# Kernel tuning notes

Hardware: AMD Instinct MI355X
Metric: run time of the kernel (lower is better)

Reference implementation:

```python
import jax, jax.numpy as jnp
import numpy as np


def _gelu(x):
    return jax.nn.gelu(x, approximate=False)


def _conv2d(x, w, b, pad=0, dil=1, groups=1):
    y = jax.lax.conv_general_dilated(
        x, w, (1, 1), [(pad, pad), (pad, pad)], rhs_dilation=(dil, dil),
        dimension_numbers=('NCHW', 'OIHW', 'NCHW'), feature_group_count=groups)
    return y + b[None, :, None, None]


def _ln_last(x, g, b, eps=1e-5):
    m = jnp.mean(x, -1, keepdims=True)
    v = jnp.var(x, -1, keepdims=True)
    return (x - m) * jax.lax.rsqrt(v + eps) * g + b


def _ln2d(x, g, b, eps=1e-5):
    # LayerNorm over channel dim of NCHW
    m = jnp.mean(x, 1, keepdims=True)
    v = jnp.var(x, 1, keepdims=True)
    return (x - m) * jax.lax.rsqrt(v + eps) * g[None, :, None, None] + b[None, :, None, None]


def _bilinear(x, py, px):
    # x: [B,C,H,W]; py,px: [B,H,W] float sample coords; zero outside
    B, C, H, W = x.shape
    y0 = jnp.floor(py)
    x0 = jnp.floor(px)
    wy = py - y0
    wx = px - x0
    xf = x.reshape(B, C, H * W)

    def g(yi, xi):
        valid = ((yi >= 0) & (yi < H) & (xi >= 0) & (xi < W)).astype(x.dtype)
        yc = jnp.clip(yi, 0, H - 1).astype(jnp.int32)
        xc = jnp.clip(xi, 0, W - 1).astype(jnp.int32)
        idx = (yc * W + xc).reshape(B, 1, H * W)
        v = jnp.take_along_axis(xf, idx, axis=2).reshape(B, C, H, W)
        return v * valid[:, None]

    return (g(y0, x0) * ((1 - wy) * (1 - wx))[:, None]
            + g(y0, x0 + 1) * ((1 - wy) * wx)[:, None]
            + g(y0 + 1, x0) * (wy * (1 - wx))[:, None]
            + g(y0 + 1, x0 + 1) * (wy * wx)[:, None])


def _deform_dw(x, ow, ob, w, b, dil):
    # modulated deformable depthwise 3x3 conv, offset_groups=1
    B, C, H, W = x.shape
    pad = dil
    off = _conv2d(x, ow, ob, pad=pad, dil=dil)          # [B,27,H,W]
    ox, oy, m = jnp.split(off, 3, axis=1)               # each [B,9,H,W]
    m = jax.nn.sigmoid(m)
    ys = jnp.arange(H, dtype=x.dtype)[None, :, None]
    xs = jnp.arange(W, dtype=x.dtype)[None, None, :]
    acc = jnp.zeros_like(x)
    for ki in range(3):
        for kj in range(3):
            kk = ki * 3 + kj
            py = ys - pad + ki * dil + oy[:, kk]
            px = xs - pad + kj * dil + ox[:, kk]
            s = _bilinear(x, py, px)                    # [B,C,H,W]
            acc = acc + s * m[:, kk][:, None] * w[:, 0, ki, kj][None, :, None, None]
    return acc + b[None, :, None, None]


def _forward(image_embed, inter_prototypes, intra_prototypes, masks,
             proj_w, proj_b, lin_w, lin_b, tok_g, tok_b, alpha,
             in_w, in_b, off0_w, off0_b, dw0_w, dw0_b,
             off1_w, off1_b, dw1_w, dw1_b, cv_w, cv_b, ln_g, ln_b,
             op0_w, op0_b, op1_w, op1_b, op2_w, op2_b,
             out0_w, out0_b, out1_w, out1_b):
    C = image_embed.shape[1]
    scale = C ** -0.5
    # prototype tokens [B,Q,C]
    pt = jnp.einsum('bqc,bnc->bqn', inter_prototypes, intra_prototypes)
    t = jnp.concatenate([inter_prototypes, pt], axis=-1) @ proj_w + proj_b
    t = _gelu(t) @ lin_w + lin_b
    t = _ln_last(t, tok_g, tok_b)
    # mask gating of image features
    pe = jnp.einsum('bnc,bnhw->bchw', intra_prototypes, masks)
    img = image_embed * pe + image_embed
    # DeformAttn
    x = _gelu(_conv2d(img, in_w, in_b))
    a = _deform_dw(x, off0_w, off0_b, dw0_w, dw0_b, dil=1)
    a = _deform_dw(a, off1_w, off1_b, dw1_w, dw1_b, dil=3)
    a = _conv2d(a, cv_w, cv_b)
    x = x * a + img
    x = _ln2d(x, ln_g, ln_b)
    y = _conv2d(x, op0_w, op0_b)
    y = _gelu(_conv2d(y, op1_w, op1_b, pad=1, groups=C))
    y = _conv2d(y, op2_w, op2_b)
    dense = y + x
    # prototype cross-attention over 8 tokens
    attn = jnp.einsum('bchw,bqc->bqhw', dense, t) * scale
    attn = jax.nn.softmax(attn, axis=1)
    attn = jnp.einsum('bqhw,bqc->bchw', attn, t)
    attn = attn + dense * alpha[None, :, None, None]
    o = _gelu(_conv2d(attn, out0_w, out0_b))
    o = _conv2d(o, out1_w, out1_b)
    return o


def setup_inputs():
    key = jax.random.key(0)
    ks = jax.random.split(key, 40)
    B, C, H, W, Q, N = 16, 256, 64, 64, 8, 9
    f32 = jnp.float32

    def rn(k, shp, s=1.0):
        return jax.random.normal(k, shp, f32) * s

    inp = {
        'image_embed': rn(ks[0], (B, C, H, W)),
        'inter_prototypes': rn(ks[1], (B, Q, C)),
        'intra_prototypes': rn(ks[2], (B, N, C)),
        'masks': jax.random.uniform(ks[3], (B, N, H, W), f32),
        'proj_w': rn(ks[4], (C + N, C), 0.02), 'proj_b': jnp.zeros((C,), f32),
        'lin_w': rn(ks[5], (C, C), 0.02), 'lin_b': jnp.zeros((C,), f32),
        'tok_g': 1.0 + rn(ks[6], (C,), 0.05), 'tok_b': rn(ks[7], (C,), 0.05),
        'alpha': jnp.ones((C,), f32) * 0.001,
        'in_w': rn(ks[8], (C, C, 1, 1), 0.02), 'in_b': jnp.zeros((C,), f32),
        'off0_w': rn(ks[9], (27, C, 3, 3), 0.01), 'off0_b': rn(ks[10], (27,), 0.01),
        'dw0_w': rn(ks[11], (C, 1, 3, 3), 0.2), 'dw0_b': jnp.zeros((C,), f32),
        'off1_w': rn(ks[12], (27, C, 3, 3), 0.01), 'off1_b': rn(ks[13], (27,), 0.01),
        'dw1_w': rn(ks[14], (C, 1, 3, 3), 0.2), 'dw1_b': jnp.zeros((C,), f32),
        'cv_w': rn(ks[15], (C, C, 1, 1), 0.02), 'cv_b': jnp.zeros((C,), f32),
        'ln_g': 1.0 + rn(ks[16], (C,), 0.05), 'ln_b': rn(ks[17], (C,), 0.05),
        'op0_w': rn(ks[18], (C, C, 1, 1), 0.02), 'op0_b': jnp.zeros((C,), f32),
        'op1_w': rn(ks[19], (C, 1, 3, 3), 0.2), 'op1_b': jnp.zeros((C,), f32),
        'op2_w': rn(ks[20], (C, C, 1, 1), 0.02), 'op2_b': jnp.zeros((C,), f32),
        'out0_w': rn(ks[21], (C // 2, C, 1, 1), 0.02), 'out0_b': jnp.zeros((C // 2,), f32),
        'out1_w': rn(ks[22], (C, C // 2, 1, 1), 0.02), 'out1_b': jnp.zeros((C,), f32),
    }
    return inp


def reference(image_embed, inter_prototypes, intra_prototypes, masks,
              proj_w, proj_b, lin_w, lin_b, tok_g, tok_b, alpha,
              in_w, in_b, off0_w, off0_b, dw0_w, dw0_b,
              off1_w, off1_b, dw1_w, dw1_b, cv_w, cv_b, ln_g, ln_b,
              op0_w, op0_b, op1_w, op1_b, op2_w, op2_b,
              out0_w, out0_b, out1_w, out1_b):
    return _forward(image_embed, inter_prototypes, intra_prototypes, masks,
                    proj_w, proj_b, lin_w, lin_b, tok_g, tok_b, alpha,
                    in_w, in_b, off0_w, off0_b, dw0_w, dw0_b,
                    off1_w, off1_b, dw1_w, dw1_b, cv_w, cv_b, ln_g, ln_b,
                    op0_w, op0_b, op1_w, op1_b, op2_w, op2_b,
                    out0_w, out0_b, out1_w, out1_b)
```

## Files before the change

### kernel.cpp

```cpp
#include <hip/hip_runtime.h>
#include <math.h>

#define BB 16
#define CC 256
#define HH 64
#define WW 64
#define HWs 4096
#define PP 65536
#define QQ 8
#define NN 9

typedef _Float16 half8_t __attribute__((ext_vector_type(8)));
typedef _Float16 half4_t __attribute__((ext_vector_type(4)));
typedef _Float16 half2_t __attribute__((ext_vector_type(2)));
typedef float floatx4 __attribute__((ext_vector_type(4)));

__device__ __forceinline__ float gelu_f(float x) {
    return 0.5f * x * (1.0f + erff(x * 0.70710678118654752f));
}

__global__ void prep_weights_kernel(const float* __restrict__ off0_w, const float* __restrict__ off1_w,
                                    const float* __restrict__ dw0_w, const float* __restrict__ dw1_w,
                                    const float* __restrict__ op1_w,
                                    const float* __restrict__ in_w, const float* __restrict__ cv_w,
                                    const float* __restrict__ op0_w, const float* __restrict__ op2_w,
                                    const float* __restrict__ out0_w, const float* __restrict__ out1_w,
                                    float* __restrict__ dwt0, float* __restrict__ dwt1,
                                    float* __restrict__ op1t,
                                    _Float16* __restrict__ wh_in, _Float16* __restrict__ wh_cv,
                                    _Float16* __restrict__ wh_op0, _Float16* __restrict__ wh_op2,
                                    _Float16* __restrict__ wh_out0, _Float16* __restrict__ wh_out1,
                                    _Float16* __restrict__ whoff0, _Float16* __restrict__ whoff1) {
    int i = blockIdx.x * 256 + threadIdx.x;
    if (i < 9*256) {
        int c = i & 255;
        int tap = i >> 8;
        dwt0[i] = dw0_w[c*9 + tap];
        dwt1[i] = dw1_w[c*9 + tap];
        op1t[i] = op1_w[c*9 + tap];
    }
    if (i < 65536) {
        wh_in[i]  = (_Float16)in_w[i];
        wh_cv[i]  = (_Float16)cv_w[i];
        wh_op0[i] = (_Float16)op0_w[i];
        wh_op2[i] = (_Float16)op2_w[i];
    }
    if (i < 32768) {
        wh_out0[i] = (_Float16)out0_w[i];
        wh_out1[i] = (_Float16)out1_w[i];
    }
    if (i < 9*32*256) {
        int ci = i & 255;
        int k32 = (i >> 8) & 31;
        int tap = i >> 13;
        float v0 = 0.f, v1 = 0.f;
        if (k32 < 27) {
            v0 = off0_w[(k32*256 + ci)*9 + tap];
            v1 = off1_w[(k32*256 + ci)*9 + tap];
        }
        whoff0[i] = (_Float16)v0;
        whoff1[i] = (_Float16)v1;
    }
}

__global__ void token_kernel(const float* __restrict__ inter, const float* __restrict__ intra,
                             const float* __restrict__ proj_w, const float* __restrict__ proj_b,
                             const float* __restrict__ lin_w, const float* __restrict__ lin_b,
                             const float* __restrict__ tok_g, const float* __restrict__ tok_b,
                             float* __restrict__ t_out) {
    int bq = blockIdx.x;
    int b = bq >> 3, q = bq & 7;
    int c = threadIdx.x;
    __shared__ float inter_s[256];
    __shared__ float pt_s[9];
    __shared__ float g_s[256];
    __shared__ float red[256];
    __shared__ float stat[2];
    inter_s[c] = inter[(b*QQ + q)*CC + c];
    __syncthreads();
    for (int n = 0; n < 9; n++) {
        red[c] = inter_s[c] * intra[(b*NN + n)*CC + c];
        __syncthreads();
        for (int s = 128; s > 0; s >>= 1) {
            if (c < s) red[c] += red[c + s];
            __syncthreads();
        }
        if (c == 0) pt_s[n] = red[0];
        __syncthreads();
    }
    float u = proj_b[c];
    for (int k = 0; k < 256; k++) u += inter_s[k] * proj_w[k*CC + c];
    for (int n = 0; n < 9; n++) u += pt_s[n] * proj_w[(256 + n)*CC + c];
    g_s[c] = gelu_f(u);
    __syncthreads();
    float v = lin_b[c];
    for (int k = 0; k < 256; k++) v += g_s[k] * lin_w[k*CC + c];
    red[c] = v;
    __syncthreads();
    for (int s = 128; s > 0; s >>= 1) { if (c < s) red[c] += red[c + s]; __syncthreads(); }
    if (c == 0) stat[0] = red[0] * (1.0f/256.0f);
    __syncthreads();
    float m = stat[0];
    red[c] = (v - m)*(v - m);
    __syncthreads();
    for (int s = 128; s > 0; s >>= 1) { if (c < s) red[c] += red[c + s]; __syncthreads(); }
    if (c == 0) stat[1] = red[0] * (1.0f/256.0f);
    __syncthreads();
    float var = stat[1];
    float r = rsqrtf(var + 1e-5f);
    t_out[(b*QQ + q)*CC + c] = (v - m) * r * tok_g[c] + tok_b[c];
}

__global__ void img_pe_kernel(const float* __restrict__ ie, const float* __restrict__ intra,
                              const float* __restrict__ masks, _Float16* __restrict__ img) {
    int b = blockIdx.z;
    int c0 = blockIdx.y * 32;
    int s0 = blockIdx.x * 32;
    __shared__ float tile[32][33];
    __shared__ float intra_s[9][32];
    __shared__ float mask_s[9][32];
    int tx = threadIdx.x, ty = threadIdx.y;
    int t = ty*32 + tx;
    for (int i = t; i < 288; i += 256) {
        int n = i >> 5, j = i & 31;
        intra_s[n][j] = intra[(b*NN + n)*CC + c0 + j];
        mask_s[n][j]  = masks[(b*NN + n)*HWs + s0 + j];
    }
    __syncthreads();
    #pragma unroll
    for (int r = 0; r < 4; r++) {
        int cl = ty + 8*r;
        float val = ie[(b*CC + c0 + cl)*HWs + s0 + tx];
        float pe = 0.f;
        #pragma unroll
        for (int n = 0; n < 9; n++) pe += intra_s[n][cl] * mask_s[n][tx];
        tile[cl][tx] = val * (1.0f + pe);
    }
    __syncthreads();
    #pragma unroll
    for (int r = 0; r < 4; r++) {
        int sl = ty + 8*r;
        img[(b*HWs + s0 + sl)*CC + c0 + tx] = (_Float16)tile[tx][sl];
    }
}

template<int CI, int CO, int ACT, int RES, int OUT>
__global__ void __launch_bounds__(256) conv1x1_mfma(const _Float16* __restrict__ in, const _Float16* __restrict__ Wh,
        const float* __restrict__ bias, const _Float16* __restrict__ res, float* __restrict__ out,
        _Float16* __restrict__ outh) {
    constexpr int KS = CI/32;
    constexpr int NF = CO/64;
    constexpr int LDR = CI + 8;
    __shared__ __align__(16) _Float16 a_lds[64*LDR];
    int t = threadIdx.x;
    int wid = t >> 6, lane = t & 63;
    int quad = lane >> 4, l16 = lane & 15;
    int p0 = blockIdx.x * 64;
    {
        const half8_t* inh = (const half8_t*)in + (size_t)p0*(CI/8);
        for (int i = t; i < 64*(CI/8); i += 256) {
            int r = i/(CI/8), c8 = i%(CI/8);
            *(half8_t*)&a_lds[r*LDR + c8*8] = inh[i];
        }
    }
    __syncthreads();
    int n0 = wid*(CO/4);
    floatx4 acc[4][NF];
    #pragma unroll
    for (int mf = 0; mf < 4; mf++)
        #pragma unroll
        for (int nf = 0; nf < NF; nf++)
            #pragma unroll
            for (int r = 0; r < 4; r++) acc[mf][nf][r] = 0.f;
    for (int ks = 0; ks < KS; ks++) {
        int k = ks*32 + quad*8;
        half8_t a[4];
        #pragma unroll
        for (int mf = 0; mf < 4; mf++)
            a[mf] = *(const half8_t*)&a_lds[(mf*16 + l16)*LDR + k];
        half8_t bfr[NF];
        #pragma unroll
        for (int nf = 0; nf < NF; nf++) {
            int brow = n0 + l16*NF + nf;
            bfr[nf] = *(const half8_t*)&Wh[(size_t)brow*CI + k];
        }
        #pragma unroll
        for (int mf = 0; mf < 4; mf++)
            #pragma unroll
            for (int nf = 0; nf < NF; nf++)
                acc[mf][nf] = __builtin_amdgcn_mfma_f32_16x16x32_f16(a[mf], bfr[nf], acc[mf][nf], 0, 0, 0);
    }
    int cb = n0 + l16*NF;
    float bs[NF];
    #pragma unroll
    for (int j = 0; j < NF; j++) bs[j] = bias[cb + j];
    #pragma unroll
    for (int mf = 0; mf < 4; mf++) {
        #pragma unroll
        for (int r = 0; r < 4; r++) {
            int p = p0 + mf*16 + quad*4 + r;
            half4_t rh;
            if (RES == 2 && NF == 4) rh = *(const half4_t*)&res[(size_t)p*CO + cb];
            _Float16 tmp[NF];
            #pragma unroll
            for (int j = 0; j < NF; j++) {
                float v = acc[mf][j][r] + bs[j];
                if (ACT) v = gelu_f(v);
                if (RES == 2 && NF == 4) v += (float)rh[j];
                tmp[j] = (_Float16)v;
            }
            if (NF == 4) {
                half4_t o4; o4[0]=tmp[0]; o4[1]=tmp[1]; o4[2]=tmp[2]; o4[3]=tmp[3];
                *(half4_t*)&outh[(size_t)p*CO + cb] = o4;
            } else {
                half2_t o2; o2[0]=tmp[0]; o2[1]=tmp[1];
                *(half2_t*)&outh[(size_t)p*CO + cb] = o2;
            }
        }
    }
}

__global__ void __launch_bounds__(256) conv_cv_ln_kernel(const _Float16* __restrict__ in, const _Float16* __restrict__ Wh,
        const float* __restrict__ bias, const _Float16* __restrict__ X, const _Float16* __restrict__ IMG,
        const float* __restrict__ g, const float* __restrict__ bb2, _Float16* __restrict__ out) {
    constexpr int CI = 256, KS = 8, LDR = 264;
    __shared__ __align__(16) _Float16 a_lds[64*LDR];
    __shared__ float rs[64][4];
    __shared__ float rs2[64][4];
    __shared__ float st[64][2];
    int t = threadIdx.x;
    int wid = t >> 6, lane = t & 63;
    int quad = lane >> 4, l16 = lane & 15;
    int p0 = blockIdx.x * 64;
    {
        const half8_t* inh = (const half8_t*)in + (size_t)p0*32;
        for (int i = t; i < 2048; i += 256) {
            int r = i >> 5, c8 = i & 31;
            *(half8_t*)&a_lds[r*LDR + c8*8] = inh[i];
        }
    }
    __syncthreads();
    int n0 = wid*64;
    floatx4 acc[4][4];
    #pragma unroll
    for (int mf = 0; mf < 4; mf++)
        #pragma unroll
        for (int nf = 0; nf < 4; nf++)
            #pragma unroll
            for (int r = 0; r < 4; r++) acc[mf][nf][r] = 0.f;
    for (int ks = 0; ks < KS; ks++) {
        int k = ks*32 + quad*8;
        half8_t a[4];
        #pragma unroll
        for (int mf = 0; mf < 4; mf++)
            a[mf] = *(const half8_t*)&a_lds[(mf*16 + l16)*LDR + k];
        half8_t bfr[4];
        #pragma unroll
        for (int nf = 0; nf < 4; nf++)
            bfr[nf] = *(const half8_t*)&Wh[(size_t)(n0 + l16*4 + nf)*CI + k];
        #pragma unroll
        for (int mf = 0; mf < 4; mf++)
            #pragma unroll
            for (int nf = 0; nf < 4; nf++)
                acc[mf][nf] = __builtin_amdgcn_mfma_f32_16x16x32_f16(a[mf], bfr[nf], acc[mf][nf], 0, 0, 0);
    }
    int cb = n0 + l16*4;
    float bs[4];
    #pragma unroll
    for (int j = 0; j < 4; j++) bs[j] = bias[cb + j];
    #pragma unroll
    for (int mf = 0; mf < 4; mf++) {
        #pragma unroll
        for (int r = 0; r < 4; r++) {
            int px_l = mf*16 + quad*4 + r;
            size_t off = (size_t)(p0 + px_l)*256 + cb;
            half4_t xh = *(const half4_t*)&X[off];
            half4_t ih = *(const half4_t*)&IMG[off];
            float s = 0.f, s2 = 0.f;
            #pragma unroll
            for (int j = 0; j < 4; j++) {
                float v = acc[mf][j][r] + bs[j];
                v = (float)xh[j]*v + (float)ih[j];
                acc[mf][j][r] = v;
                s += v; s2 += v*v;
            }
            s += __shfl_xor(s, 1); s2 += __shfl_xor(s2, 1);
            s += __shfl_xor(s, 2); s2 += __shfl_xor(s2, 2);
            s += __shfl_xor(s, 4); s2 += __shfl_xor(s2, 4);
            s += __shfl_xor(s, 8); s2 += __shfl_xor(s2, 8);
            if (l16 == 0) { rs[px_l][wid] = s; rs2[px_l][wid] = s2; }
        }
    }
    __syncthreads();
    if (t < 64) {
        float m = 0.f, q = 0.f;
        #pragma unroll
        for (int w = 0; w < 4; w++) { m += rs[t][w]; q += rs2[t][w]; }
        m *= (1.0f/256.0f);
        float var = q*(1.0f/256.0f) - m*m;
        st[t][0] = m;
        st[t][1] = rsqrtf(var + 1e-5f);
    }
    __syncthreads();
    float ga[4], ba[4];
    #pragma unroll
    for (int j = 0; j < 4; j++) { ga[j] = g[cb + j]; ba[j] = bb2[cb + j]; }
    #pragma unroll
    for (int mf = 0; mf < 4; mf++) {
        #pragma unroll
        for (int r = 0; r < 4; r++) {
            int px_l = mf*16 + quad*4 + r;
            float m = st[px_l][0];
            float ri = st[px_l][1];
            half4_t o4;
            #pragma unroll
            for (int j = 0; j < 4; j++)
                o4[j] = (_Float16)((acc[mf][j][r] - m)*ri*ga[j] + ba[j]);
            *(half4_t*)&out[(size_t)(p0 + px_l)*256 + cb] = o4;
        }
    }
}

template<int DIL>
__global__ void __launch_bounds__(256) off_conv_mfma(const _Float16* __restrict__ x, const _Float16* __restrict__ Wh,
        const float* __restrict__ bias, float* __restrict__ off) {
    constexpr int LDR = 264;
    __shared__ __align__(16) _Float16 xs[70*LDR];
    int raw = blockIdx.x;
    int bh = (raw & 7) * 128 + (raw >> 3);
    int b = bh >> 6, h = bh & 63;
    int t = threadIdx.x;
    int wid = t >> 6, lane = t & 63;
    int quad = lane >> 4, l16 = lane & 15;
    for (int i = t; i < 6*LDR; i += 256) {
        int r = i/LDR, c = i%LDR;
        int row = (r < 3) ? r : (64 + r);
        xs[row*LDR + c] = (_Float16)0.f;
    }
    floatx4 acc[2];
    #pragma unroll
    for (int nf = 0; nf < 2; nf++)
        #pragma unroll
        for (int r = 0; r < 4; r++) acc[nf][r] = 0.f;
    for (int ki = 0; ki < 3; ki++) {
        int hrow = h + (ki - 1)*DIL;
        __syncthreads();
        if (hrow >= 0 && hrow < 64) {
            const half8_t* row = (const half8_t*)(x + ((size_t)(b*64 + hrow)*64) * 256);
            for (int i = t; i < 2048; i += 256) {
                int r = i >> 5, c8 = i & 31;
                *(half8_t*)&xs[(r + 3)*LDR + c8*8] = row[r*32 + c8];
            }
        } else {
            half8_t z = (half8_t)((_Float16)0.f);
            for (int i = t; i < 2048; i += 256) {
                int r = i >> 5, c8 = i & 31;
                *(half8_t*)&xs[(r + 3)*LDR + c8*8] = z;
            }
        }
        __syncthreads();
        #pragma unroll
        for (int kj = 0; kj < 3; kj++) {
            const _Float16* wt = Wh + (size_t)(ki*3 + kj)*32*256;
            int wrow = wid*16 + l16 + (kj - 1)*DIL + 3;
            #pragma unroll
            for (int cs = 0; cs < 8; cs++) {
                int k = cs*32 + quad*8;
                half8_t a = *(const half8_t*)&xs[wrow*LDR + k];
                half8_t b0 = *(const half8_t*)&wt[(size_t)l16*256 + k];
                half8_t b1 = *(const half8_t*)&wt[(size_t)(16 + l16)*256 + k];
                acc[0] = __builtin_amdgcn_mfma_f32_16x16x32_f16(a, b0, acc[0], 0, 0, 0);
                acc[1] = __builtin_amdgcn_mfma_f32_16x16x32_f16(a, b1, acc[1], 0, 0, 0);
            }
        }
    }
    int pbase = (b*64 + h)*64;
    #pragma unroll
    for (int nf = 0; nf < 2; nf++) {
        int kcol = nf*16 + l16;
        if (kcol < 27) {
            float bs = bias[kcol];
            #pragma unroll
            for (int r = 0; r < 4; r++) {
                int w = wid*16 + quad*4 + r;
                off[(size_t)(pbase + w)*27 + kcol] = acc[nf][r] + bs;
            }
        }
    }
}

template<int DIL>
__global__ void __launch_bounds__(256) deform_kernel(const _Float16* __restrict__ src, const float* __restrict__ off,
        const float* __restrict__ dwt, const float* __restrict__ dwb, _Float16* __restrict__ out) {
    int raw = blockIdx.x;
    int swz = (raw & 7) * 512 + (raw >> 3);
    int wq = swz & 3;
    int bh = swz >> 2;
    int b = bh >> 6, h = bh & 63;
    int t = threadIdx.x;
    int c4 = t & 63;
    int ps = t >> 6;

    __shared__ float4 wq4[144];
    __shared__ int4   iq4[144];
    __shared__ float  dw_lds[9*256];

    for (int i = t; i < 9*256; i += 256) dw_lds[i] = dwt[i];

    for (int j = t; j < 144; j += 256) {
        int lw = j / 9;
        int kk = j - lw*9;
        int w = wq*16 + lw;
        int p = (b*64 + h)*64 + w;
        const float* op = off + (size_t)p*27;
        float ox = op[kk];
        float oy = op[9 + kk];
        float mm = op[18 + kk];
        mm = 1.0f / (1.0f + expf(-mm));
        int ki = kk / 3, kj = kk - ki*3;
        float py = (float)(h - DIL + ki*DIL) + oy;
        float px = (float)(w - DIL + kj*DIL) + ox;
        float y0f = floorf(py), x0f = floorf(px);
        float wy = py - y0f, wx = px - x0f;
        int y0 = (int)y0f, x0 = (int)x0f;
        int y1 = y0 + 1, x1 = x0 + 1;
        float w00 = (1.f - wy)*(1.f - wx)*mm;
        float w01 = (1.f - wy)*wx*mm;
        float w10 = wy*(1.f - wx)*mm;
        float w11 = wy*wx*mm;
        bool yv0 = (y0 >= 0) && (y0 < 64);
        bool yv1 = (y1 >= 0) && (y1 < 64);
        bool xv0 = (x0 >= 0) && (x0 < 64);
        bool xv1 = (x1 >= 0) && (x1 < 64);
        int y0c = min(max(y0, 0), 63), y1c = min(max(y1, 0), 63);
        int x0c = min(max(x0, 0), 63), x1c = min(max(x1, 0), 63);
        int base = b*4096;
        float4 wv;
        wv.x = (yv0 && xv0) ? w00 : 0.f;
        wv.y = (yv0 && xv1) ? w01 : 0.f;
        wv.z = (yv1 && xv0) ? w10 : 0.f;
        wv.w = (yv1 && xv1) ? w11 : 0.f;
        wq4[j] = wv;
        int4 iv;
        iv.x = (base + y0c*64 + x0c) << 9;
        iv.y = (base + y0c*64 + x1c) << 9;
        iv.z = (base + y1c*64 + x0c) << 9;
        iv.w = (base + y1c*64 + x1c) << 9;
        iq4[j] = iv;
    }
    __syncthreads();

    float4 bv = ((const float4*)dwb)[c4];
    const char* srcb = (const char*)src + (size_t)c4*8;
    for (int i = 0; i < 4; i++) {
        int lw = ps*4 + i;
        int jb = lw*9;
        int w = wq*16 + lw;
        int p = (b*64 + h)*64 + w;
        half4_t v[9][4];
        #pragma unroll
        for (int kk = 0; kk < 9; kk++) {
            int4 iv = iq4[jb + kk];
            int o0 = __builtin_amdgcn_readfirstlane(iv.x);
            int o1 = __builtin_amdgcn_readfirstlane(iv.y);
            int o2 = __builtin_amdgcn_readfirstlane(iv.z);
            int o3 = __builtin_amdgcn_readfirstlane(iv.w);
            v[kk][0] = *(const half4_t*)(srcb + o0);
            v[kk][1] = *(const half4_t*)(srcb + o1);
            v[kk][2] = *(const half4_t*)(srcb + o2);
            v[kk][3] = *(const half4_t*)(srcb + o3);
        }
        __builtin_amdgcn_sched_barrier(0);
        float4 acc = make_float4(0.f,0.f,0.f,0.f);
        #pragma unroll
        for (int kk = 0; kk < 9; kk++) {
            float4 wv = wq4[jb + kk];
            float4 dw = ((const float4*)dw_lds)[kk*64 + c4];
            float sx = (float)v[kk][0][0]*wv.x + (float)v[kk][1][0]*wv.y + (float)v[kk][2][0]*wv.z + (float)v[kk][3][0]*wv.w;
            float sy = (float)v[kk][0][1]*wv.x + (float)v[kk][1][1]*wv.y + (float)v[kk][2][1]*wv.z + (float)v[kk][3][1]*wv.w;
            float sz = (float)v[kk][0][2]*wv.x + (float)v[kk][1][2]*wv.y + (float)v[kk][2][2]*wv.z + (float)v[kk][3][2]*wv.w;
            float sw = (float)v[kk][0][3]*wv.x + (float)v[kk][1][3]*wv.y + (float)v[kk][2][3]*wv.z + (float)v[kk][3][3]*wv.w;
            acc.x += sx * dw.x;
            acc.y += sy * dw.y;
            acc.z += sz * dw.z;
            acc.w += sw * dw.w;
        }
        half4_t o4;
        o4[0] = (_Float16)(acc.x + bv.x);
        o4[1] = (_Float16)(acc.y + bv.y);
        o4[2] = (_Float16)(acc.z + bv.z);
        o4[3] = (_Float16)(acc.w + bv.w);
        ((half4_t*)out)[(size_t)p*64 + c4] = o4;
    }
}

__global__ void __launch_bounds__(256) dw3x3_kernel(const _Float16* __restrict__ in, const float* __restrict__ wt,
        const float* __restrict__ bias, _Float16* __restrict__ out) {
    int raw = blockIdx.x;
    int swz = (raw & 7) * 2048 + (raw >> 3);
    int gid = swz*256 + threadIdx.x;
    int c4 = gid & 63;
    int p = gid >> 6;
    int w = p & 63;
    int h = (p >> 6) & 63;
    int b = p >> 12;
    float4 acc = ((const float4*)bias)[c4];
    #pragma unroll
    for (int ki = 0; ki < 3; ki++) {
        int hh = h + ki - 1;
        if (hh < 0 || hh >= 64) continue;
        #pragma unroll
        for (int kj = 0; kj < 3; kj++) {
            int wwp = w + kj - 1;
            if (wwp < 0 || wwp >= 64) continue;
            half4_t v = ((const half4_t*)in)[((b*64 + hh)*64 + wwp)*64 + c4];
            float4 wv = ((const float4*)wt)[(ki*3 + kj)*64 + c4];
            acc.x += (float)v[0]*wv.x; acc.y += (float)v[1]*wv.y;
            acc.z += (float)v[2]*wv.z; acc.w += (float)v[3]*wv.w;
        }
    }
    half4_t o4;
    o4[0] = (_Float16)gelu_f(acc.x);
    o4[1] = (_Float16)gelu_f(acc.y);
    o4[2] = (_Float16)gelu_f(acc.z);
    o4[3] = (_Float16)gelu_f(acc.w);
    ((half4_t*)out)[p*64 + c4] = o4;
}

__global__ void __launch_bounds__(256) attn_out_fused(const _Float16* __restrict__ dense,
        const float* __restrict__ tok, const float* __restrict__ alpha,
        const _Float16* __restrict__ W0, const float* __restrict__ b0,
        const _Float16* __restrict__ W1, const float* __restrict__ b1,
        float* __restrict__ out) {
    __shared__ __align__(16) _Float16 d_att[64*264];
    __shared__ __align__(16) _Float16 t_q[16*264];
    __shared__ __align__(16) _Float16 t_t[256*32];
    __shared__ __align__(16) _Float16 w_lds[64*40];
    __shared__ __align__(16) _Float16 o0_lds[64*136];
    __shared__ float al_s[256];
    int t = threadIdx.x;
    int wid = t >> 6, lane = t & 63;
    int quad = lane >> 4, l16 = lane & 15;
    int p0 = blockIdx.x * 64;
    int b = p0 >> 12;

    for (int i = t; i < 16*264; i += 256) t_q[i] = (_Float16)0.f;
    for (int i = t; i < 256*32; i += 256) t_t[i] = (_Float16)0.f;
    for (int i = t; i < 64*40;  i += 256) w_lds[i] = (_Float16)0.f;
    __syncthreads();

    const half8_t* dh = (const half8_t*)dense + (size_t)p0*32;
    for (int i = t; i < 2048; i += 256) {
        int r = i >> 5, c8 = i & 31;
        *(half8_t*)&d_att[r*264 + c8*8] = dh[i];
    }
    for (int i = t; i < 512; i += 256) {
        int q = i >> 6, j = i & 63;
        float4 tv = ((const float4*)tok)[(b*8 + q)*64 + j];
        int c0 = j*4;
        t_q[q*264 + c0 + 0] = (_Float16)tv.x;
        t_q[q*264 + c0 + 1] = (_Float16)tv.y;
        t_q[q*264 + c0 + 2] = (_Float16)tv.z;
        t_q[q*264 + c0 + 3] = (_Float16)tv.w;
        t_t[(c0 + 0)*32 + q] = (_Float16)tv.x;
        t_t[(c0 + 1)*32 + q] = (_Float16)tv.y;
        t_t[(c0 + 2)*32 + q] = (_Float16)tv.z;
        t_t[(c0 + 3)*32 + q] = (_Float16)tv.w;
    }
    al_s[t] = alpha[t];
    __syncthreads();

    floatx4 s4;
    s4[0]=0.f; s4[1]=0.f; s4[2]=0.f; s4[3]=0.f;
    #pragma unroll
    for (int ks = 0; ks < 8; ks++) {
        int k = ks*32 + quad*8;
        half8_t a = *(const half8_t*)&d_att[(wid*16 + l16)*264 + k];
        half8_t bf = *(const half8_t*)&t_q[l16*264 + k];
        s4 = __builtin_amdgcn_mfma_f32_16x16x32_f16(a, bf, s4, 0, 0, 0);
    }
    float wgt[4];
    #pragma unroll
    for (int r = 0; r < 4; r++) {
        float sc = s4[r] * 0.0625f;
        float mx = sc;
        mx = fmaxf(mx, __shfl_xor(mx, 1));
        mx = fmaxf(mx, __shfl_xor(mx, 2));
        mx = fmaxf(mx, __shfl_xor(mx, 4));
        float e = expf(sc - mx);
        float dn = e;
        dn += __shfl_xor(dn, 1);
        dn += __shfl_xor(dn, 2);
        dn += __shfl_xor(dn, 4);
        wgt[r] = e / dn;
    }
    if (l16 < 8) {
        #pragma unroll
        for (int r = 0; r < 4; r++)
            w_lds[(wid*16 + quad*4 + r)*40 + l16] = (_Float16)wgt[r];
    }
    __syncthreads();

    half8_t aw = *(const half8_t*)&w_lds[(wid*16 + l16)*40 + quad*8];
    floatx4 z4; z4[0]=0.f; z4[1]=0.f; z4[2]=0.f; z4[3]=0.f;
    floatx4 acc2[16];
    #pragma unroll
    for (int nf = 0; nf < 16; nf++) {
        half8_t bf = *(const half8_t*)&t_t[(l16*16 + nf)*32 + quad*8];
        acc2[nf] = __builtin_amdgcn_mfma_f32_16x16x32_f16(aw, bf, z4, 0, 0, 0);
    }
    int cb = l16*16;
    float alv[16];
    #pragma unroll
    for (int nf = 0; nf < 16; nf++) alv[nf] = al_s[cb + nf];
    #pragma unroll
    for (int r = 0; r < 4; r++) {
        int px = wid*16 + quad*4 + r;
        half8_t dlo = *(const half8_t*)&d_att[px*264 + cb];
        half8_t dhi = *(const half8_t*)&d_att[px*264 + cb + 8];
        half8_t olo, ohi;
        #pragma unroll
        for (int nf = 0; nf < 8; nf++) {
            olo[nf] = (_Float16)(acc2[nf][r]     + (float)dlo[nf]*alv[nf]);
            ohi[nf] = (_Float16)(acc2[nf + 8][r] + (float)dhi[nf]*alv[nf + 8]);
        }
        *(half8_t*)&d_att[px*264 + cb] = olo;
        *(half8_t*)&d_att[px*264 + cb + 8] = ohi;
    }
    __syncthreads();

    int n0 = wid*32;
    floatx4 acc0[4][2];
    #pragma unroll
    for (int mf = 0; mf < 4; mf++)
        #pragma unroll
        for (int nf = 0; nf < 2; nf++)
            #pragma unroll
            for (int r = 0; r < 4; r++) acc0[mf][nf][r] = 0.f;
    #pragma unroll
    for (int ks = 0; ks < 8; ks++) {
        int k = ks*32 + quad*8;
        half8_t a[4];
        #pragma unroll
        for (int mf = 0; mf < 4; mf++)
            a[mf] = *(const half8_t*)&d_att[(mf*16 + l16)*264 + k];
        half8_t bf[2];
        #pragma unroll
        for (int nf = 0; nf < 2; nf++)
            bf[nf] = *(const half8_t*)&W0[(size_t)(n0 + l16*2 + nf)*256 + k];
        #pragma unroll
        for (int mf = 0; mf < 4; mf++)
            #pragma unroll
            for (int nf = 0; nf < 2; nf++)
                acc0[mf][nf] = __builtin_amdgcn_mfma_f32_16x16x32_f16(a[mf], bf[nf], acc0[mf][nf], 0, 0, 0);
    }
    int cb0 = n0 + l16*2;
    float bs0[2] = { b0[cb0], b0[cb0 + 1] };
    #pragma unroll
    for (int mf = 0; mf < 4; mf++) {
        #pragma unroll
        for (int r = 0; r < 4; r++) {
            int px = mf*16 + quad*4 + r;
            half2_t o2;
            o2[0] = (_Float16)gelu_f(acc0[mf][0][r] + bs0[0]);
            o2[1] = (_Float16)gelu_f(acc0[mf][1][r] + bs0[1]);
            *(half2_t*)&o0_lds[px*136 + cb0] = o2;
        }
    }
    __syncthreads();

    int n1 = wid*64;
    floatx4 acc1[4][4];
    #pragma unroll
    for (int mf = 0; mf < 4; mf++)
        #pragma unroll
        for (int nf = 0; nf < 4; nf++)
            #pragma unroll
            for (int r = 0; r < 4; r++) acc1[mf][nf][r] = 0.f;
    #pragma unroll
    for (int ks = 0; ks < 4; ks++) {
        int k = ks*32 + quad*8;
        half8_t a[4];
        #pragma unroll
        for (int mf = 0; mf < 4; mf++)
            a[mf] = *(const half8_t*)&o0_lds[(mf*16 + l16)*136 + k];
        half8_t bf[4];
        #pragma unroll
        for (int nf = 0; nf < 4; nf++)
            bf[nf] = *(const half8_t*)&W1[(size_t)(n1 + nf*16 + l16)*128 + k];
        #pragma unroll
        for (int mf = 0; mf < 4; mf++)
            #pragma unroll
            for (int nf = 0; nf < 4; nf++)
                acc1[mf][nf] = __builtin_amdgcn_mfma_f32_16x16x32_f16(a[mf], bf[nf], acc1[mf][nf], 0, 0, 0);
    }
    size_t bb = (size_t)b * ((size_t)CC * HWs) + (size_t)(p0 & 4095);
    #pragma unroll
    for (int nf = 0; nf < 4; nf++) {
        int co = n1 + nf*16 + l16;
        float bs = b1[co];
        #pragma unroll
        for (int mf = 0; mf < 4; mf++) {
            float4 vst;
            vst.x = acc1[mf][nf][0] + bs;
            vst.y = acc1[mf][nf][1] + bs;
            vst.z = acc1[mf][nf][2] + bs;
            vst.w = acc1[mf][nf][3] + bs;
            *(float4*)&out[bb + (size_t)co*HWs + mf*16 + quad*4] = vst;
        }
    }
}

extern "C" void kernel_launch(void* const* d_in, const int* in_sizes, int n_in,
                              void* d_out, int out_size, void* d_ws, size_t ws_size,
                              hipStream_t stream) {
    const float* image_embed = (const float*)d_in[0];
    const float* inter_p     = (const float*)d_in[1];
    const float* intra_p     = (const float*)d_in[2];
    const float* masks       = (const float*)d_in[3];
    const float* proj_w      = (const float*)d_in[4];
    const float* proj_b      = (const float*)d_in[5];
    const float* lin_w       = (const float*)d_in[6];
    const float* lin_b       = (const float*)d_in[7];
    const float* tok_g       = (const float*)d_in[8];
    const float* tok_b       = (const float*)d_in[9];
    const float* alpha       = (const float*)d_in[10];
    const float* in_w        = (const float*)d_in[11];
    const float* in_b        = (const float*)d_in[12];
    const float* off0_w      = (const float*)d_in[13];
    const float* off0_b      = (const float*)d_in[14];
    const float* dw0_w       = (const float*)d_in[15];
    const float* dw0_b       = (const float*)d_in[16];
    const float* off1_w      = (const float*)d_in[17];
    const float* off1_b      = (const float*)d_in[18];
    const float* dw1_w       = (const float*)d_in[19];
    const float* dw1_b       = (const float*)d_in[20];
    const float* cv_w        = (const float*)d_in[21];
    const float* cv_b        = (const float*)d_in[22];
    const float* ln_g        = (const float*)d_in[23];
    const float* ln_b        = (const float*)d_in[24];
    const float* op0_w       = (const float*)d_in[25];
    const float* op0_b       = (const float*)d_in[26];
    const float* op1_w       = (const float*)d_in[27];
    const float* op1_b       = (const float*)d_in[28];
    const float* op2_w       = (const float*)d_in[29];
    const float* op2_b       = (const float*)d_in[30];
    const float* out0_w      = (const float*)d_in[31];
    const float* out0_b      = (const float*)d_in[32];
    const float* out1_w      = (const float*)d_in[33];
    const float* out1_b      = (const float*)d_in[34];
    (void)ws_size; (void)in_sizes; (void)n_in; (void)out_size;

    float* ws = (float*)d_ws;
    const size_t BIG = (size_t)PP * CC;
    float* A   = ws;
    float* Bb  = A + BIG;
    float* Cb  = Bb + BIG;
    float* OFF = Cb + BIG;
    float* TOK = OFF + (size_t)PP*27;
    float* DWT0 = TOK + BB*QQ*CC;
    float* DWT1 = DWT0 + 9*256;
    float* OP1T = DWT1 + 9*256;
    _Float16* WH_IN   = (_Float16*)(OP1T + 9*256);
    _Float16* WH_CV   = WH_IN + 65536;
    _Float16* WH_OP0  = WH_CV + 65536;
    _Float16* WH_OP2  = WH_OP0 + 65536;
    _Float16* WH_OUT0 = WH_OP2 + 65536;
    _Float16* WH_OUT1 = WH_OUT0 + 32768;
    _Float16* WHOFF0  = WH_OUT1 + 32768;
    _Float16* WHOFF1  = WHOFF0 + 9*32*256;
    _Float16* IMGH = (_Float16*)A;
    _Float16* Y0H  = (_Float16*)A;
    _Float16* Y1H  = Y0H + (size_t)PP*CC;
    _Float16* XH   = (_Float16*)Bb;
    _Float16* A1H  = XH + (size_t)PP*CC;
    _Float16* A2H  = (_Float16*)Cb;
    _Float16* DENH = (_Float16*)Cb;
    _Float16* XLNH = (_Float16*)d_out;

    prep_weights_kernel<<<(9*32*256 + 255)/256, 256, 0, stream>>>(
        off0_w, off1_w, dw0_w, dw1_w, op1_w,
        in_w, cv_w, op0_w, op2_w, out0_w, out1_w,
        DWT0, DWT1, OP1T,
        WH_IN, WH_CV, WH_OP0, WH_OP2, WH_OUT0, WH_OUT1, WHOFF0, WHOFF1);
    token_kernel<<<BB*QQ, 256, 0, stream>>>(inter_p, intra_p, proj_w, proj_b,
                                            lin_w, lin_b, tok_g, tok_b, TOK);
    img_pe_kernel<<<dim3(HWs/32, CC/32, BB), dim3(32,8), 0, stream>>>(image_embed, intra_p, masks, IMGH);
    conv1x1_mfma<256,256,1,0,1><<<PP/64, 256, 0, stream>>>(IMGH, WH_IN, in_b, nullptr, nullptr, XH);
    off_conv_mfma<1><<<BB*HH, 256, 0, stream>>>(XH, WHOFF0, off0_b, OFF);
    deform_kernel<1><<<BB*HH*4, 256, 0, stream>>>(XH, OFF, DWT0, dw0_b, A1H);
    off_conv_mfma<3><<<BB*HH, 256, 0, stream>>>(A1H, WHOFF1, off1_b, OFF);
    deform_kernel<3><<<BB*HH*4, 256, 0, stream>>>(A1H, OFF, DWT1, dw1_b, A2H);
    conv_cv_ln_kernel<<<PP/64, 256, 0, stream>>>(A2H, WH_CV, cv_b, XH, IMGH, ln_g, ln_b, XLNH);
    conv1x1_mfma<256,256,0,0,1><<<PP/64, 256, 0, stream>>>(XLNH, WH_OP0, op0_b, nullptr, nullptr, Y0H);
    dw3x3_kernel<<<PP*64/256, 256, 0, stream>>>(Y0H, OP1T, op1_b, Y1H);
    conv1x1_mfma<256,256,0,2,1><<<PP/64, 256, 0, stream>>>(Y1H, WH_OP2, op2_b, XLNH, nullptr, DENH);
    attn_out_fused<<<PP/64, 256, 0, stream>>>(DENH, TOK, alpha,
                                              WH_OUT0, out0_b, WH_OUT1, out1_b, (float*)d_out);
}
```

Before: 776.9 us.

## Double-buffer deform gathers and shrink attn_out shared memory footprint

The deform kernel now handles half a row (32 pixels) per block instead of a quarter. Each thread processes 8 pixels, and gathers for the next pixel are issued into a second register buffer while the current one is consumed, so memory latency overlaps with compute. Launch bounds request 2 blocks per CU. The attn_out kernel aliases o0_lds onto the t_q region and halves the t_t row stride, which cuts its LDS footprint to allow more occupancy. The cost is doubled gather registers in deform, which may cause spilling, and fewer blocks per launch.

```diff
diff --git a/kernel.cpp b/kernel.cpp
--- a/kernel.cpp
+++ b/kernel.cpp
@@ -390,27 +390,27 @@
 }
 
 template<int DIL>
-__global__ void __launch_bounds__(256) deform_kernel(const _Float16* __restrict__ src, const float* __restrict__ off,
+__global__ void __launch_bounds__(256, 2) deform_kernel(const _Float16* __restrict__ src, const float* __restrict__ off,
         const float* __restrict__ dwt, const float* __restrict__ dwb, _Float16* __restrict__ out) {
     int raw = blockIdx.x;
-    int swz = (raw & 7) * 512 + (raw >> 3);
-    int wq = swz & 3;
-    int bh = swz >> 2;
+    int swz = (raw & 7) * 256 + (raw >> 3);
+    int whalf = swz & 1;
+    int bh = swz >> 1;
     int b = bh >> 6, h = bh & 63;
     int t = threadIdx.x;
     int c4 = t & 63;
     int ps = t >> 6;
 
-    __shared__ float4 wq4[144];
-    __shared__ int4   iq4[144];
+    __shared__ float4 wq4[288];
+    __shared__ int4   iq4[288];
     __shared__ float  dw_lds[9*256];
 
     for (int i = t; i < 9*256; i += 256) dw_lds[i] = dwt[i];
 
-    for (int j = t; j < 144; j += 256) {
+    for (int j = t; j < 288; j += 256) {
         int lw = j / 9;
         int kk = j - lw*9;
-        int w = wq*16 + lw;
+        int w = whalf*32 + lw;
         int p = (b*64 + h)*64 + w;
         const float* op = off + (size_t)p*27;
         float ox = op[kk];
@@ -451,13 +451,14 @@
     __syncthreads();
 
     float4 bv = ((const float4*)dwb)[c4];
-    const char* srcb = (const char*)src + (size_t)c4*8;
-    for (int i = 0; i < 4; i++) {
-        int lw = ps*4 + i;
+    const char* srcc = (const char*)src;
+    int c4b = c4*8;
+    int pbase = (b*64 + h)*64 + whalf*32;
+
+    half4_t vA[9][4], vB[9][4];
+
+    auto LOADS_A = [&](int lw) {
         int jb = lw*9;
-        int w = wq*16 + lw;
-        int p = (b*64 + h)*64 + w;
-        half4_t v[9][4];
         #pragma unroll
         for (int kk = 0; kk < 9; kk++) {
             int4 iv = iq4[jb + kk];
@@ -465,21 +466,38 @@
             int o1 = __builtin_amdgcn_readfirstlane(iv.y);
             int o2 = __builtin_amdgcn_readfirstlane(iv.z);
             int o3 = __builtin_amdgcn_readfirstlane(iv.w);
-            v[kk][0] = *(const half4_t*)(srcb + o0);
-            v[kk][1] = *(const half4_t*)(srcb + o1);
-            v[kk][2] = *(const half4_t*)(srcb + o2);
-            v[kk][3] = *(const half4_t*)(srcb + o3);
-        }
-        __builtin_amdgcn_sched_barrier(0);
+            vA[kk][0] = *(const half4_t*)(srcc + (unsigned)(o0 + c4b));
+            vA[kk][1] = *(const half4_t*)(srcc + (unsigned)(o1 + c4b));
+            vA[kk][2] = *(const half4_t*)(srcc + (unsigned)(o2 + c4b));
+            vA[kk][3] = *(const half4_t*)(srcc + (unsigned)(o3 + c4b));
+        }
+    };
+    auto LOADS_B = [&](int lw) {
+        int jb = lw*9;
+        #pragma unroll
+        for (int kk = 0; kk < 9; kk++) {
+            int4 iv = iq4[jb + kk];
+            int o0 = __builtin_amdgcn_readfirstlane(iv.x);
+            int o1 = __builtin_amdgcn_readfirstlane(iv.y);
+            int o2 = __builtin_amdgcn_readfirstlane(iv.z);
+            int o3 = __builtin_amdgcn_readfirstlane(iv.w);
+            vB[kk][0] = *(const half4_t*)(srcc + (unsigned)(o0 + c4b));
+            vB[kk][1] = *(const half4_t*)(srcc + (unsigned)(o1 + c4b));
+            vB[kk][2] = *(const half4_t*)(srcc + (unsigned)(o2 + c4b));
+            vB[kk][3] = *(const half4_t*)(srcc + (unsigned)(o3 + c4b));
+        }
+    };
+    auto CONSUME_A = [&](int lw) {
+        int jb = lw*9;
         float4 acc = make_float4(0.f,0.f,0.f,0.f);
         #pragma unroll
         for (int kk = 0; kk < 9; kk++) {
             float4 wv = wq4[jb + kk];
             float4 dw = ((const float4*)dw_lds)[kk*64 + c4];
-            float sx = (float)v[kk][0][0]*wv.x + (float)v[kk][1][0]*wv.y + (float)v[kk][2][0]*wv.z + (float)v[kk][3][0]*wv.w;
-            float sy = (float)v[kk][0][1]*wv.x + (float)v[kk][1][1]*wv.y + (float)v[kk][2][1]*wv.z + (float)v[kk][3][1]*wv.w;
-            float sz = (float)v[kk][0][2]*wv.x + (float)v[kk][1][2]*wv.y + (float)v[kk][2][2]*wv.z + (float)v[kk][3][2]*wv.w;
-            float sw = (float)v[kk][0][3]*wv.x + (float)v[kk][1][3]*wv.y + (float)v[kk][2][3]*wv.z + (float)v[kk][3][3]*wv.w;
+            float sx = (float)vA[kk][0][0]*wv.x + (float)vA[kk][1][0]*wv.y + (float)vA[kk][2][0]*wv.z + (float)vA[kk][3][0]*wv.w;
+            float sy = (float)vA[kk][0][1]*wv.x + (float)vA[kk][1][1]*wv.y + (float)vA[kk][2][1]*wv.z + (float)vA[kk][3][1]*wv.w;
+            float sz = (float)vA[kk][0][2]*wv.x + (float)vA[kk][1][2]*wv.y + (float)vA[kk][2][2]*wv.z + (float)vA[kk][3][2]*wv.w;
+            float sw = (float)vA[kk][0][3]*wv.x + (float)vA[kk][1][3]*wv.y + (float)vA[kk][2][3]*wv.z + (float)vA[kk][3][3]*wv.w;
             acc.x += sx * dw.x;
             acc.y += sy * dw.y;
             acc.z += sz * dw.z;
@@ -490,7 +508,45 @@
         o4[1] = (_Float16)(acc.y + bv.y);
         o4[2] = (_Float16)(acc.z + bv.z);
         o4[3] = (_Float16)(acc.w + bv.w);
-        ((half4_t*)out)[(size_t)p*64 + c4] = o4;
+        ((half4_t*)out)[(size_t)(pbase + lw)*64 + c4] = o4;
+    };
+    auto CONSUME_B = [&](int lw) {
+        int jb = lw*9;
+        float4 acc = make_float4(0.f,0.f,0.f,0.f);
+        #pragma unroll
+        for (int kk = 0; kk < 9; kk++) {
+            float4 wv = wq4[jb + kk];
+            float4 dw = ((const float4*)dw_lds)[kk*64 + c4];
+            float sx = (float)vB[kk][0][0]*wv.x + (float)vB[kk][1][0]*wv.y + (float)vB[kk][2][0]*wv.z + (float)vB[kk][3][0]*wv.w;
+            float sy = (float)vB[kk][0][1]*wv.x + (float)vB[kk][1][1]*wv.y + (float)vB[kk][2][1]*wv.z + (float)vB[kk][3][1]*wv.w;
+            float sz = (float)vB[kk][0][2]*wv.x + (float)vB[kk][1][2]*wv.y + (float)vB[kk][2][2]*wv.z + (float)vB[kk][3][2]*wv.w;
+            float sw = (float)vB[kk][0][3]*wv.x + (float)vB[kk][1][3]*wv.y + (float)vB[kk][2][3]*wv.z + (float)vB[kk][3][3]*wv.w;
+            acc.x += sx * dw.x;
+            acc.y += sy * dw.y;
+            acc.z += sz * dw.z;
+            acc.w += sw * dw.w;
+        }
+        half4_t o4;
+        o4[0] = (_Float16)(acc.x + bv.x);
+        o4[1] = (_Float16)(acc.y + bv.y);
+        o4[2] = (_Float16)(acc.z + bv.z);
+        o4[3] = (_Float16)(acc.w + bv.w);
+        ((half4_t*)out)[(size_t)(pbase + lw)*64 + c4] = o4;
+    };
+
+    int lw0 = ps*8;
+    LOADS_A(lw0);
+    __builtin_amdgcn_sched_barrier(0);
+    #pragma unroll
+    for (int ii = 0; ii < 4; ii++) {
+        LOADS_B(lw0 + 2*ii + 1);
+        __builtin_amdgcn_sched_barrier(0);
+        CONSUME_A(lw0 + 2*ii);
+        if (ii < 3) {
+            LOADS_A(lw0 + 2*ii + 2);
+            __builtin_amdgcn_sched_barrier(0);
+        }
+        CONSUME_B(lw0 + 2*ii + 1);
     }
 }
 
@@ -532,21 +588,20 @@
         const _Float16* __restrict__ W0, const float* __restrict__ b0,
         const _Float16* __restrict__ W1, const float* __restrict__ b1,
         float* __restrict__ out) {
-    __shared__ __align__(16) _Float16 d_att[64*264];
-    __shared__ __align__(16) _Float16 t_q[16*264];
-    __shared__ __align__(16) _Float16 t_t[256*32];
-    __shared__ __align__(16) _Float16 w_lds[64*40];
-    __shared__ __align__(16) _Float16 o0_lds[64*136];
+    __shared__ __align__(16) _Float16 smem[16896 + 10880];
     __shared__ float al_s[256];
+    _Float16* d_att = smem;
+    _Float16* t_q   = smem + 16896;
+    _Float16* t_t   = t_q + 4224;
+    _Float16* w_lds = t_t + 4096;
+    _Float16* o0_lds = t_q;
     int t = threadIdx.x;
     int wid = t >> 6, lane = t & 63;
     int quad = lane >> 4, l16 = lane & 15;
     int p0 = blockIdx.x * 64;
     int b = p0 >> 12;
 
-    for (int i = t; i < 16*264; i += 256) t_q[i] = (_Float16)0.f;
-    for (int i = t; i < 256*32; i += 256) t_t[i] = (_Float16)0.f;
-    for (int i = t; i < 64*40;  i += 256) w_lds[i] = (_Float16)0.f;
+    for (int i = t; i < 10880; i += 256) t_q[i] = (_Float16)0.f;
     __syncthreads();
 
     const half8_t* dh = (const half8_t*)dense + (size_t)p0*32;
@@ -562,10 +617,10 @@
         t_q[q*264 + c0 + 1] = (_Float16)tv.y;
         t_q[q*264 + c0 + 2] = (_Float16)tv.z;
         t_q[q*264 + c0 + 3] = (_Float16)tv.w;
-        t_t[(c0 + 0)*32 + q] = (_Float16)tv.x;
-        t_t[(c0 + 1)*32 + q] = (_Float16)tv.y;
-        t_t[(c0 + 2)*32 + q] = (_Float16)tv.z;
-        t_t[(c0 + 3)*32 + q] = (_Float16)tv.w;
+        t_t[(c0 + 0)*16 + q] = (_Float16)tv.x;
+        t_t[(c0 + 1)*16 + q] = (_Float16)tv.y;
+        t_t[(c0 + 2)*16 + q] = (_Float16)tv.z;
+        t_t[(c0 + 3)*16 + q] = (_Float16)tv.w;
     }
     al_s[t] = alpha[t];
     __syncthreads();
@@ -606,7 +661,7 @@
     floatx4 acc2[16];
     #pragma unroll
     for (int nf = 0; nf < 16; nf++) {
-        half8_t bf = *(const half8_t*)&t_t[(l16*16 + nf)*32 + quad*8];
+        half8_t bf = *(const half8_t*)&t_t[(l16*16 + nf)*16 + quad*8];
         acc2[nf] = __builtin_amdgcn_mfma_f32_16x16x32_f16(aw, bf, z4, 0, 0, 0);
     }
     int cb = l16*16;
@@ -788,9 +843,9 @@
     img_pe_kernel<<<dim3(HWs/32, CC/32, BB), dim3(32,8), 0, stream>>>(image_embed, intra_p, masks, IMGH);
     conv1x1_mfma<256,256,1,0,1><<<PP/64, 256, 0, stream>>>(IMGH, WH_IN, in_b, nullptr, nullptr, XH);
     off_conv_mfma<1><<<BB*HH, 256, 0, stream>>>(XH, WHOFF0, off0_b, OFF);
-    deform_kernel<1><<<BB*HH*4, 256, 0, stream>>>(XH, OFF, DWT0, dw0_b, A1H);
+    deform_kernel<1><<<BB*HH*2, 256, 0, stream>>>(XH, OFF, DWT0, dw0_b, A1H);
     off_conv_mfma<3><<<BB*HH, 256, 0, stream>>>(A1H, WHOFF1, off1_b, OFF);
-    deform_kernel<3><<<BB*HH*4, 256, 0, stream>>>(A1H, OFF, DWT1, dw1_b, A2H);
+    deform_kernel<3><<<BB*HH*2, 256, 0, stream>>>(A1H, OFF, DWT1, dw1_b, A2H);
     conv_cv_ln_kernel<<<PP/64, 256, 0, stream>>>(A2H, WH_CV, cv_b, XH, IMGH, ln_g, ln_b, XLNH);
     conv1x1_mfma<256,256,0,0,1><<<PP/64, 256, 0, stream>>>(XLNH, WH_OP0, op0_b, nullptr, nullptr, Y0H);
     dw3x3_kernel<<<PP*64/256, 256, 0, stream>>>(Y0H, OP1T, op1_b, Y1H);
```

After: 862.8 us. +11.1%, slower.
